# Kernel optimization log

Measured on AMD Instinct MI355X. Metric: run time of the kernel, lower is better.

The kernel has to match this reference:

```python
import jax, jax.numpy as jnp
import numpy as np

W_BIT = 8

def quantize_weight(w, k=W_BIT):
    # DoReFa-style weight quantization (conv2d_Q_fn): tanh-normalize to [0,1],
    # uniform-quantize to 2^k-1 levels (round with straight-through), map to [-1,1].
    n = float(2 ** k - 1)
    t = jnp.tanh(w)
    t = t / (2.0 * jnp.max(jnp.abs(t))) + 0.5
    q = t + jax.lax.stop_gradient(jnp.round(t * n) / n - t)
    return 2.0 * q - 1.0

def qconv(x, w, b, pad):
    wq = quantize_weight(w)
    y = jax.lax.conv_general_dilated(
        x, wq, window_strides=(1, 1), padding=[(pad, pad), (pad, pad)],
        dimension_numbers=('NCHW', 'OIHW', 'NCHW'))
    return y + b[None, :, None, None]

def upsample2x(x):
    # nearest-neighbor, scale_factor=2
    return jnp.repeat(jnp.repeat(x, 2, axis=2), 2, axis=3)

def setup_inputs() -> dict:
    key = jax.random.key(0)
    ks = jax.random.split(key, 11)
    F = 256
    C3 = jax.random.normal(ks[0], (8, 512, 64, 64), dtype=jnp.float32)
    C4 = jax.random.normal(ks[1], (8, 1024, 32, 32), dtype=jnp.float32)
    C5 = jax.random.normal(ks[2], (8, 2048, 16, 16), dtype=jnp.float32)
    # conv params (torch nn.Conv2d default has bias)
    w5 = jax.random.normal(ks[3], (F, 2048, 1, 1), dtype=jnp.float32) * 0.02
    b5 = jax.random.normal(ks[4], (F,), dtype=jnp.float32) * 0.01
    w4 = jax.random.normal(ks[5], (F, 1024, 1, 1), dtype=jnp.float32) * 0.02
    b4 = jax.random.normal(ks[6], (F,), dtype=jnp.float32) * 0.01
    w3 = jax.random.normal(ks[7], (F, 512, 1, 1), dtype=jnp.float32) * 0.02
    b3 = jax.random.normal(ks[8], (F,), dtype=jnp.float32) * 0.01
    w3_2 = jax.random.normal(ks[9], (F, F, 3, 3), dtype=jnp.float32) * 0.02
    b3_2 = jax.random.normal(ks[10], (F,), dtype=jnp.float32) * 0.01
    return {"C3": C3, "C4": C4, "C5": C5,
            "w5": w5, "b5": b5, "w4": w4, "b4": b4,
            "w3": w3, "b3": b3, "w3_2": w3_2, "b3_2": b3_2}

def reference(C3, C4, C5, w5, b5, w4, b4, w3, b3, w3_2, b3_2):
    P5_x = qconv(C5, w5, b5, pad=0)            # [B,256,16,16]
    P5_up = upsample2x(P5_x)                   # [B,256,32,32]
    P4_x = qconv(C4, w4, b4, pad=0) + P5_up    # [B,256,32,32]
    P4_up = upsample2x(P4_x)                   # [B,256,64,64]
    P3_x = qconv(C3, w3, b3, pad=0) + P4_up    # [B,256,64,64]
    P3_x = qconv(P3_x, w3_2, b3_2, pad=1)      # [B,256,64,64]
    return P3_x
```

## Files before the change

### kernel.cpp

```cpp
#include <hip/hip_runtime.h>
#include <stdint.h>

typedef unsigned short u16;
typedef short s16x8 __attribute__((ext_vector_type(8)));
typedef short s16x4 __attribute__((ext_vector_type(4)));
typedef float f32x4 __attribute__((ext_vector_type(4)));
typedef unsigned int u32x4 __attribute__((ext_vector_type(4)));

__device__ __forceinline__ u16 f2bf(float x) {
    unsigned u = __float_as_uint(x);
    unsigned r = u + 0x7FFFu + ((u >> 16) & 1u);
    return (u16)(r >> 16);
}
__device__ __forceinline__ float bf2f(u16 h) {
    return __uint_as_float((unsigned)h << 16);
}

__device__ __forceinline__ void gll16(void* lds, const void* g) {
    __builtin_amdgcn_global_load_lds(
        (const __attribute__((address_space(1))) void*)g,
        (__attribute__((address_space(3))) void*)lds,
        16, 0, 0);
}

__global__ __launch_bounds__(256) void reduce_maxabs(
    const float* __restrict__ a0, int n0, const float* __restrict__ a1, int n1,
    const float* __restrict__ a2, int n2, const float* __restrict__ a3, int n3,
    float* __restrict__ out) {
    int which = blockIdx.y;
    const float* w = which == 0 ? a0 : which == 1 ? a1 : which == 2 ? a2 : a3;
    int n = which == 0 ? n0 : which == 1 ? n1 : which == 2 ? n2 : n3;
    float m = 0.f;
    for (int i = blockIdx.x * 256 + threadIdx.x; i < n; i += gridDim.x * 256)
        m = fmaxf(m, fabsf(w[i]));
#pragma unroll
    for (int off = 32; off > 0; off >>= 1)
        m = fmaxf(m, __shfl_down(m, off, 64));
    __shared__ float sm[4];
    if ((threadIdx.x & 63) == 0) sm[threadIdx.x >> 6] = m;
    __syncthreads();
    if (threadIdx.x == 0) {
        m = fmaxf(fmaxf(sm[0], sm[1]), fmaxf(sm[2], sm[3]));
        atomicMax((int*)out + which, __float_as_int(m));
    }
}

__global__ __launch_bounds__(256) void quant_w(
    const float* __restrict__ w5, const float* __restrict__ w4,
    const float* __restrict__ w3, const float* __restrict__ w32,
    const float* __restrict__ mx,
    u16* __restrict__ q5, u16* __restrict__ q4,
    u16* __restrict__ q3, u16* __restrict__ q2) {
    int b = blockIdx.x, t = threadIdx.x;
    int which, i;
    const float* w;
    if (b < 2048)      { which = 0; w = w5;  i = b * 256 + t; }
    else if (b < 3072) { which = 1; w = w4;  i = (b - 2048) * 256 + t; }
    else if (b < 3584) { which = 2; w = w3;  i = (b - 3072) * 256 + t; }
    else               { which = 3; w = w32; i = (b - 3584) * 256 + t; }
    float inv = 0.5f / tanhf(mx[which]);
    float tt = tanhf(w[i]) * inv + 0.5f;
    float q = rintf(tt * 255.f) * (1.f / 255.f);
    u16 o = f2bf(2.f * q - 1.f);
    if (which == 0) q5[i] = o;
    else if (which == 1) q4[i] = o;
    else if (which == 2) q3[i] = o;
    else {
        int kw = i % 3, kh = (i / 3) % 3, c = (i / 9) & 255, f = i / 2304;
        q2[(size_t)((kh * 3 + kw) * 256 + f) * 256 + c] = o;
    }
}

__global__ __launch_bounds__(256) void transpose_nhwc(
    const float* __restrict__ C5, const float* __restrict__ C4,
    const float* __restrict__ C3,
    u16* __restrict__ c5n, u16* __restrict__ c4n, u16* __restrict__ c3n) {
    __shared__ float tile[128][65];
    int t = threadIdx.x, b = blockIdx.x;
    const float* src; u16* dst; int C, HW, cb, hwb, nn;
    if (b < 512)       { nn = b >> 6; int r = b & 63; cb = r >> 2; hwb = r & 3;
                         C = 2048; HW = 256;  src = C5; dst = c5n; }
    else if (b < 1536) { int l = b - 512;  nn = l >> 7; int r = l & 127; cb = r >> 4; hwb = r & 15;
                         C = 1024; HW = 1024; src = C4; dst = c4n; }
    else               { int l = b - 1536; nn = l >> 8; int r = l & 255; cb = r >> 6; hwb = r & 63;
                         C = 512;  HW = 4096; src = C3; dst = c3n; }
    int c0 = cb << 7, hw0 = hwb << 6;
    const float* s2 = src + (size_t)nn * C * HW;
#pragma unroll
    for (int i = 0; i < 8; ++i) {
        int c = (t >> 4) + (i << 4);
        int hw = (t & 15) << 2;
        f32x4 v = *(const f32x4*)(s2 + (size_t)(c0 + c) * HW + hw0 + hw);
        tile[c][hw] = v.x; tile[c][hw + 1] = v.y; tile[c][hw + 2] = v.z; tile[c][hw + 3] = v.w;
    }
    __syncthreads();
    u16* d2 = dst + (size_t)nn * C * HW;
#pragma unroll
    for (int i = 0; i < 4; ++i) {
        int hw = (t >> 4) + (i << 4);
        int g = t & 15;
        s16x8 o;
#pragma unroll
        for (int j = 0; j < 8; ++j) o[j] = (short)f2bf(tile[8 * g + j][hw]);
        *(s16x8*)(d2 + (size_t)(hw0 + hw) * C + c0 + 8 * g) = o;
    }
}

template<int BF, int BPX, int FJ, int FI, int ATOMIC>
__global__ __launch_bounds__(256) void gemm_qconv(
    const u16* __restrict__ A, const u16* __restrict__ B,
    const float* __restrict__ bias,
    const float* __restrict__ addF, const u16* __restrict__ addB,
    float* __restrict__ outF, u16* __restrict__ outB,
    int Kfull, int Kchunk, int Wlog, int HWlog) {
    __shared__ u16 As[BF * 64];
    __shared__ u16 Bs[BPX * 64];
    int t = threadIdx.x, lane = t & 63, wv = t >> 6;
    int l16 = lane & 15, quad = lane >> 4;
    int f0 = blockIdx.y * BF, p0 = blockIdx.x * BPX;
    int wf = (wv >> 1) * (BF / 2), wp = (wv & 1) * (BPX / 2);
    f32x4 acc[FJ][FI] = {};
    const u16* Ab = A + (size_t)f0 * Kfull;
    const u16* Bb = B + (size_t)p0 * Kfull;
    int row = t >> 3, c8 = t & 7;
    int k_begin = blockIdx.z * Kchunk, k_end = k_begin + Kchunk;
    for (int k0 = k_begin; k0 < k_end; k0 += 64) {
#pragma unroll
        for (int it = 0; it < BF / 32; ++it)
            gll16(&As[(it * 256 + wv * 64) * 8], Ab + (size_t)(it * 32 + row) * Kfull + k0 + c8 * 8);
#pragma unroll
        for (int it = 0; it < BPX / 32; ++it)
            gll16(&Bs[(it * 256 + wv * 64) * 8], Bb + (size_t)(it * 32 + row) * Kfull + k0 + c8 * 8);
        __syncthreads();
#pragma unroll
        for (int kk = 0; kk < 64; kk += 32) {
            s16x8 a[FJ], b[FI];
#pragma unroll
            for (int j = 0; j < FJ; ++j)
                a[j] = *(const s16x8*)&As[(wf + 16 * j + l16) * 64 + kk + quad * 8];
#pragma unroll
            for (int i = 0; i < FI; ++i)
                b[i] = *(const s16x8*)&Bs[(wp + 16 * i + l16) * 64 + kk + quad * 8];
#pragma unroll
            for (int j = 0; j < FJ; ++j)
#pragma unroll
                for (int i = 0; i < FI; ++i)
                    acc[j][i] = __builtin_amdgcn_mfma_f32_16x16x32_bf16(a[j], b[i], acc[j][i], 0, 0, 0);
        }
        __syncthreads();
    }
    int W = 1 << Wlog;
    bool bias_on = (blockIdx.z == 0);
#pragma unroll
    for (int j = 0; j < FJ; ++j) {
        int f = f0 + wf + 16 * j + (quad << 2);
        f32x4 bz = {0.f, 0.f, 0.f, 0.f};
        if (bias_on) bz = *(const f32x4*)(bias + f);
#pragma unroll
        for (int i = 0; i < FI; ++i) {
            int px = p0 + wp + 16 * i + l16;
            f32x4 v = acc[j][i] + bz;
            if (ATOMIC) {
                float* d = outF + (size_t)px * 256 + f;
                atomicAdd(d + 0, v.x); atomicAdd(d + 1, v.y);
                atomicAdd(d + 2, v.z); atomicAdd(d + 3, v.w);
            } else {
                if (addF || addB) {
                    int n = px >> HWlog;
                    int rem = px & ((1 << HWlog) - 1);
                    int h = rem >> Wlog, ww = rem & (W - 1);
                    int sp = (n << (HWlog - 2)) + ((h >> 1) << (Wlog - 1)) + (ww >> 1);
                    if (addF) v += *(const f32x4*)(addF + (size_t)sp * 256 + f);
                    else {
                        s16x4 av = *(const s16x4*)(addB + (size_t)sp * 256 + f);
                        v.x += bf2f((u16)av.x); v.y += bf2f((u16)av.y);
                        v.z += bf2f((u16)av.z); v.w += bf2f((u16)av.w);
                    }
                }
                if (outB) {
                    s16x4 o;
                    o.x = (short)f2bf(v.x); o.y = (short)f2bf(v.y);
                    o.z = (short)f2bf(v.z); o.w = (short)f2bf(v.w);
                    *(s16x4*)(outB + (size_t)px * 256 + f) = o;
                } else {
                    *(f32x4*)(outF + (size_t)px * 256 + f) = v;
                }
            }
        }
    }
}

#define CVS 40
__global__ __launch_bounds__(256) void conv3x3_q(
    const u16* __restrict__ X, const u16* __restrict__ Wq,
    const float* __restrict__ bias, float* __restrict__ outp) {
    __shared__ u16 Rg[6 * 66 * CVS];
    int t = threadIdx.x, lane = t & 63, wv = t >> 6;
    int l16 = lane & 15, quad = lane >> 4;
    int n = blockIdx.x >> 4, h0 = (blockIdx.x & 15) << 2;
    int f0 = blockIdx.y << 6;
    f32x4 acc[4][4] = {};
    for (int c0 = 0; c0 < 256; c0 += 32) {
#pragma unroll
        for (int it = 0; it < 7; ++it) {
            int chunk = it * 256 + t;
            if (chunk < 1584) {
                int r = chunk / 264;
                int rest = chunk - r * 264;
                int w = rest >> 2, c8 = rest & 3;
                int h = h0 - 1 + r, ww = w - 1;
                u32x4 v; v.x = 0; v.y = 0; v.z = 0; v.w = 0;
                if ((unsigned)h < 64u && (unsigned)ww < 64u)
                    v = *(const u32x4*)(X + ((((size_t)n << 12) + (h << 6) + ww) << 8) + c0 + c8 * 8);
                *(u32x4*)(Rg + (r * 66 + w) * CVS + c8 * 8) = v;
            }
        }
        __syncthreads();
#pragma unroll
        for (int tp = 0; tp < 9; ++tp) {
            int dh = tp / 3, dw = tp % 3;
            s16x8 a[4], b[4];
#pragma unroll
            for (int i = 0; i < 4; ++i)
                b[i] = *(const s16x8*)(Rg + ((wv + dh) * 66 + 16 * i + l16 + dw) * CVS + quad * 8);
#pragma unroll
            for (int j = 0; j < 4; ++j)
                a[j] = *(const s16x8*)(Wq + (((size_t)tp * 256 + f0 + 16 * j + l16) << 8) + c0 + quad * 8);
#pragma unroll
            for (int j = 0; j < 4; ++j)
#pragma unroll
                for (int i = 0; i < 4; ++i)
                    acc[j][i] = __builtin_amdgcn_mfma_f32_16x16x32_bf16(a[j], b[i], acc[j][i], 0, 0, 0);
        }
        __syncthreads();
    }
    int h = h0 + wv;
#pragma unroll
    for (int j = 0; j < 4; ++j) {
        int f = f0 + 16 * j + (quad << 2);
        f32x4 bz = *(const f32x4*)(bias + f);
#pragma unroll
        for (int i = 0; i < 4; ++i) {
            int w = 16 * i + l16;
#pragma unroll
            for (int r = 0; r < 4; ++r)
                outp[((size_t)(n * 256 + f + r) << 12) + (h << 6) + w] = acc[j][i][r] + bz[r];
        }
    }
}

extern "C" void kernel_launch(void* const* d_in, const int* in_sizes, int n_in,
                              void* d_out, int out_size, void* d_ws, size_t ws_size,
                              hipStream_t stream) {
    (void)in_sizes; (void)n_in; (void)out_size; (void)ws_size;
    const float* C3  = (const float*)d_in[0];
    const float* C4  = (const float*)d_in[1];
    const float* C5  = (const float*)d_in[2];
    const float* w5  = (const float*)d_in[3];
    const float* b5  = (const float*)d_in[4];
    const float* w4  = (const float*)d_in[5];
    const float* b4  = (const float*)d_in[6];
    const float* w3  = (const float*)d_in[7];
    const float* b3  = (const float*)d_in[8];
    const float* w32 = (const float*)d_in[9];
    const float* b32 = (const float*)d_in[10];
    float* outp = (float*)d_out;

    char* p = (char*)d_ws;
    float* mx = (float*)p;  p += 256;
    u16* q5   = (u16*)p;    p += (size_t)524288 * 2;
    u16* q4   = (u16*)p;    p += (size_t)262144 * 2;
    u16* q3   = (u16*)p;    p += (size_t)131072 * 2;
    u16* q2   = (u16*)p;    p += (size_t)589824 * 2;
    u16* c5n  = (u16*)p;    p += (size_t)4194304 * 2;
    u16* c4n  = (u16*)p;    p += (size_t)8388608 * 2;
    u16* c3n  = (u16*)p;    p += (size_t)16777216 * 2;
    float* p5x = (float*)p; p += (size_t)2097152 * 4;
    u16* p4x  = (u16*)p;    p += (size_t)8388608 * 2;
    u16* p3xn = (u16*)p;    p += (size_t)8388608 * 2;

    hipMemsetAsync(mx, 0, 256, stream);
    hipMemsetAsync(p5x, 0, (size_t)2097152 * 4, stream);
    reduce_maxabs<<<dim3(128, 4), 256, 0, stream>>>(w5, 524288, w4, 262144,
                                                    w3, 131072, w32, 589824, mx);
    quant_w<<<5888, 256, 0, stream>>>(w5, w4, w3, w32, mx, q5, q4, q3, q2);
    transpose_nhwc<<<3584, 256, 0, stream>>>(C5, C4, C3, c5n, c4n, c3n);
    gemm_qconv<64, 64, 2, 2, 1><<<dim3(32, 4, 4), 256, 0, stream>>>(
        q5, c5n, b5, nullptr, nullptr, p5x, nullptr, 2048, 512, 4, 8);
    gemm_qconv<64, 128, 2, 4, 0><<<dim3(64, 4, 1), 256, 0, stream>>>(
        q4, c4n, b4, p5x, nullptr, nullptr, p4x, 1024, 1024, 5, 10);
    gemm_qconv<128, 128, 4, 4, 0><<<dim3(256, 2, 1), 256, 0, stream>>>(
        q3, c3n, b3, nullptr, p4x, nullptr, p3xn, 512, 512, 6, 12);
    conv3x3_q<<<dim3(128, 4), 256, 0, stream>>>(p3xn, q2, b32, outp);
}
```

Baseline: 351.0 us.

## Stage conv3x3 weights in LDS, replace atomic split-K with two partial buffers, rotate transpose reads

The 3x3 conv kernel now copies each chunk's weight tiles into shared memory in two phases (taps 0-4, then 5-8) instead of reading weights straight from global memory inside the MFMA loop. The P5 split-K GEMM drops from four K-chunks with atomicAdd to two chunks, each writing its own partial buffer. The P4 epilogue sums both partials, which also removes the memset. The transpose kernel rotates its LDS read order per thread group to reduce bank conflicts. The trade-offs are extra shared memory and barriers in the conv kernel, and less parallelism in the P5 GEMM.

```diff
diff --git a/kernel.cpp b/kernel.cpp
--- a/kernel.cpp
+++ b/kernel.cpp
@@ -95,24 +95,28 @@
     }
     __syncthreads();
     u16* d2 = dst + (size_t)nn * C * HW;
+    int g = t & 15;
 #pragma unroll
     for (int i = 0; i < 4; ++i) {
         int hw = (t >> 4) + (i << 4);
-        int g = t & 15;
         s16x8 o;
 #pragma unroll
-        for (int j = 0; j < 8; ++j) o[j] = (short)f2bf(tile[8 * g + j][hw]);
+        for (int jj = 0; jj < 8; ++jj) {
+            int j = (jj + g) & 7;
+            o[j] = (short)f2bf(tile[8 * g + j][hw]);
+        }
         *(s16x8*)(d2 + (size_t)(hw0 + hw) * C + c0 + 8 * g) = o;
     }
 }
 
-template<int BF, int BPX, int FJ, int FI, int ATOMIC>
+template<int BF, int BPX, int FJ, int FI>
 __global__ __launch_bounds__(256) void gemm_qconv(
     const u16* __restrict__ A, const u16* __restrict__ B,
     const float* __restrict__ bias,
-    const float* __restrict__ addF, const u16* __restrict__ addB,
+    const float* __restrict__ addF, const float* __restrict__ addF2,
+    const u16* __restrict__ addB,
     float* __restrict__ outF, u16* __restrict__ outB,
-    int Kfull, int Kchunk, int Wlog, int HWlog) {
+    int Kfull, int Kchunk, int Wlog, int HWlog, size_t zstride) {
     __shared__ u16 As[BF * 64];
     __shared__ u16 Bs[BPX * 64];
     int t = threadIdx.x, lane = t & 63, wv = t >> 6;
@@ -151,40 +155,38 @@
     }
     int W = 1 << Wlog;
     bool bias_on = (blockIdx.z == 0);
+    float* outFz = outF ? outF + blockIdx.z * zstride : outF;
 #pragma unroll
     for (int j = 0; j < FJ; ++j) {
         int f = f0 + wf + 16 * j + (quad << 2);
         f32x4 bz = {0.f, 0.f, 0.f, 0.f};
-        if (bias_on) bz = *(const f32x4*)(bias + f);
+        if (bias_on && bias) bz = *(const f32x4*)(bias + f);
 #pragma unroll
         for (int i = 0; i < FI; ++i) {
             int px = p0 + wp + 16 * i + l16;
             f32x4 v = acc[j][i] + bz;
-            if (ATOMIC) {
-                float* d = outF + (size_t)px * 256 + f;
-                atomicAdd(d + 0, v.x); atomicAdd(d + 1, v.y);
-                atomicAdd(d + 2, v.z); atomicAdd(d + 3, v.w);
+            if (addF || addB) {
+                int nn = px >> HWlog;
+                int rem = px & ((1 << HWlog) - 1);
+                int h = rem >> Wlog, ww = rem & (W - 1);
+                int sp = (nn << (HWlog - 2)) + ((h >> 1) << (Wlog - 1)) + (ww >> 1);
+                if (addF) {
+                    f32x4 s = *(const f32x4*)(addF + (size_t)sp * 256 + f);
+                    if (addF2) s += *(const f32x4*)(addF2 + (size_t)sp * 256 + f);
+                    v += s;
+                } else {
+                    s16x4 av = *(const s16x4*)(addB + (size_t)sp * 256 + f);
+                    v.x += bf2f((u16)av.x); v.y += bf2f((u16)av.y);
+                    v.z += bf2f((u16)av.z); v.w += bf2f((u16)av.w);
+                }
+            }
+            if (outB) {
+                s16x4 o;
+                o.x = (short)f2bf(v.x); o.y = (short)f2bf(v.y);
+                o.z = (short)f2bf(v.z); o.w = (short)f2bf(v.w);
+                *(s16x4*)(outB + (size_t)px * 256 + f) = o;
             } else {
-                if (addF || addB) {
-                    int n = px >> HWlog;
-                    int rem = px & ((1 << HWlog) - 1);
-                    int h = rem >> Wlog, ww = rem & (W - 1);
-                    int sp = (n << (HWlog - 2)) + ((h >> 1) << (Wlog - 1)) + (ww >> 1);
-                    if (addF) v += *(const f32x4*)(addF + (size_t)sp * 256 + f);
-                    else {
-                        s16x4 av = *(const s16x4*)(addB + (size_t)sp * 256 + f);
-                        v.x += bf2f((u16)av.x); v.y += bf2f((u16)av.y);
-                        v.z += bf2f((u16)av.z); v.w += bf2f((u16)av.w);
-                    }
-                }
-                if (outB) {
-                    s16x4 o;
-                    o.x = (short)f2bf(v.x); o.y = (short)f2bf(v.y);
-                    o.z = (short)f2bf(v.z); o.w = (short)f2bf(v.w);
-                    *(s16x4*)(outB + (size_t)px * 256 + f) = o;
-                } else {
-                    *(f32x4*)(outF + (size_t)px * 256 + f) = v;
-                }
+                *(f32x4*)(outFz + (size_t)px * 256 + f) = v;
             }
         }
     }
@@ -195,6 +197,7 @@
     const u16* __restrict__ X, const u16* __restrict__ Wq,
     const float* __restrict__ bias, float* __restrict__ outp) {
     __shared__ u16 Rg[6 * 66 * CVS];
+    __shared__ u16 Aw[5 * 64 * CVS];
     int t = threadIdx.x, lane = t & 63, wv = t >> 6;
     int l16 = lane & 15, quad = lane >> 4;
     int n = blockIdx.x >> 4, h0 = (blockIdx.x & 15) << 2;
@@ -215,9 +218,16 @@
                 *(u32x4*)(Rg + (r * 66 + w) * CVS + c8 * 8) = v;
             }
         }
-        __syncthreads();
-#pragma unroll
-        for (int tp = 0; tp < 9; ++tp) {
+#pragma unroll
+        for (int it = 0; it < 5; ++it) {
+            int chunk = it * 256 + t;
+            int tap = chunk >> 8, fr = (chunk >> 2) & 63, cc = chunk & 3;
+            *(u32x4*)(Aw + (tap * 64 + fr) * CVS + cc * 8) =
+                *(const u32x4*)(Wq + (((size_t)tap * 256 + f0 + fr) << 8) + c0 + cc * 8);
+        }
+        __syncthreads();
+#pragma unroll
+        for (int tp = 0; tp < 5; ++tp) {
             int dh = tp / 3, dw = tp % 3;
             s16x8 a[4], b[4];
 #pragma unroll
@@ -225,7 +235,32 @@
                 b[i] = *(const s16x8*)(Rg + ((wv + dh) * 66 + 16 * i + l16 + dw) * CVS + quad * 8);
 #pragma unroll
             for (int j = 0; j < 4; ++j)
-                a[j] = *(const s16x8*)(Wq + (((size_t)tp * 256 + f0 + 16 * j + l16) << 8) + c0 + quad * 8);
+                a[j] = *(const s16x8*)(Aw + (tp * 64 + 16 * j + l16) * CVS + quad * 8);
+#pragma unroll
+            for (int j = 0; j < 4; ++j)
+#pragma unroll
+                for (int i = 0; i < 4; ++i)
+                    acc[j][i] = __builtin_amdgcn_mfma_f32_16x16x32_bf16(a[j], b[i], acc[j][i], 0, 0, 0);
+        }
+        __syncthreads();
+#pragma unroll
+        for (int it = 0; it < 4; ++it) {
+            int chunk = it * 256 + t;
+            int tap = 5 + (chunk >> 8), fr = (chunk >> 2) & 63, cc = chunk & 3;
+            *(u32x4*)(Aw + ((tap - 5) * 64 + fr) * CVS + cc * 8) =
+                *(const u32x4*)(Wq + (((size_t)tap * 256 + f0 + fr) << 8) + c0 + cc * 8);
+        }
+        __syncthreads();
+#pragma unroll
+        for (int tp = 5; tp < 9; ++tp) {
+            int dh = tp / 3, dw = tp % 3;
+            s16x8 a[4], b[4];
+#pragma unroll
+            for (int i = 0; i < 4; ++i)
+                b[i] = *(const s16x8*)(Rg + ((wv + dh) * 66 + 16 * i + l16 + dw) * CVS + quad * 8);
+#pragma unroll
+            for (int j = 0; j < 4; ++j)
+                a[j] = *(const s16x8*)(Aw + ((tp - 5) * 64 + 16 * j + l16) * CVS + quad * 8);
 #pragma unroll
             for (int j = 0; j < 4; ++j)
 #pragma unroll
@@ -275,21 +310,24 @@
     u16* c5n  = (u16*)p;    p += (size_t)4194304 * 2;
     u16* c4n  = (u16*)p;    p += (size_t)8388608 * 2;
     u16* c3n  = (u16*)p;    p += (size_t)16777216 * 2;
-    float* p5x = (float*)p; p += (size_t)2097152 * 4;
+    float* p5xa = (float*)p; p += (size_t)2097152 * 4;
+    float* p5xb = (float*)p; p += (size_t)2097152 * 4;
     u16* p4x  = (u16*)p;    p += (size_t)8388608 * 2;
     u16* p3xn = (u16*)p;    p += (size_t)8388608 * 2;
 
     hipMemsetAsync(mx, 0, 256, stream);
-    hipMemsetAsync(p5x, 0, (size_t)2097152 * 4, stream);
     reduce_maxabs<<<dim3(128, 4), 256, 0, stream>>>(w5, 524288, w4, 262144,
                                                     w3, 131072, w32, 589824, mx);
     quant_w<<<5888, 256, 0, stream>>>(w5, w4, w3, w32, mx, q5, q4, q3, q2);
     transpose_nhwc<<<3584, 256, 0, stream>>>(C5, C4, C3, c5n, c4n, c3n);
-    gemm_qconv<64, 64, 2, 2, 1><<<dim3(32, 4, 4), 256, 0, stream>>>(
-        q5, c5n, b5, nullptr, nullptr, p5x, nullptr, 2048, 512, 4, 8);
-    gemm_qconv<64, 128, 2, 4, 0><<<dim3(64, 4, 1), 256, 0, stream>>>(
-        q4, c4n, b4, p5x, nullptr, nullptr, p4x, 1024, 1024, 5, 10);
-    gemm_qconv<128, 128, 4, 4, 0><<<dim3(256, 2, 1), 256, 0, stream>>>(
-        q3, c3n, b3, nullptr, p4x, nullptr, p3xn, 512, 512, 6, 12);
+    gemm_qconv<64, 64, 2, 2><<<dim3(32, 4, 2), 256, 0, stream>>>(
+        q5, c5n, b5, nullptr, nullptr, nullptr, p5xa, nullptr,
+        2048, 1024, 4, 8, (size_t)2097152);
+    gemm_qconv<64, 128, 2, 4><<<dim3(64, 4, 1), 256, 0, stream>>>(
+        q4, c4n, b4, p5xa, p5xb, nullptr, nullptr, p4x,
+        1024, 1024, 5, 10, 0);
+    gemm_qconv<128, 128, 4, 4><<<dim3(256, 2, 1), 256, 0, stream>>>(
+        q3, c3n, b3, nullptr, nullptr, p4x, nullptr, p3xn,
+        512, 512, 6, 12, 0);
     conv3x3_q<<<dim3(128, 4), 256, 0, stream>>>(p3xn, q2, b32, outp);
 }
```

Result: faster. 292.5 us (-16.7%).
